# Kernel optimization log

Measured on AMD Instinct MI355X. Metric: run time of the kernel, lower is better.

Reference implementation:

```python
import jax, jax.numpy as jnp
import numpy as np

B, D, H, DOUT, E, K = 8192, 1024, 4096, 1024, 8, 2


def setup_inputs() -> dict:
    key = jax.random.key(0)
    ks = jax.random.split(key, 7)
    s_d = 1.0 / np.sqrt(D)
    s_h = 1.0 / np.sqrt(H)
    return {
        "x": jax.random.normal(ks[0], (B, D), jnp.float32),
        "Wg": jax.random.uniform(ks[1], (D, E), jnp.float32, -s_d, s_d),
        "bg": jax.random.uniform(ks[2], (E,), jnp.float32, -s_d, s_d),
        "W1": jax.random.uniform(ks[3], (E, D, H), jnp.float32, -s_d, s_d),
        "b1": jax.random.uniform(ks[4], (E, H), jnp.float32, -s_d, s_d),
        "W2": jax.random.uniform(ks[5], (E, H, DOUT), jnp.float32, -s_h, s_h),
        "b2": jax.random.uniform(ks[6], (E, DOUT), jnp.float32, -s_h, s_h),
    }


def reference(x, Wg, bg, W1, b1, W2, b2):
    # gating
    gate_probs = jax.nn.softmax(x @ Wg + bg, axis=-1)          # [B, E]
    top_k_probs, top_k_idx = jax.lax.top_k(gate_probs, K)       # [B, K]
    top_k_probs = top_k_probs / jnp.sum(top_k_probs, axis=-1, keepdims=True)

    # dense all-expert compute (faithful to torch.stack over experts)
    h = jax.nn.gelu(jnp.einsum('bd,edh->beh', x, W1) + b1, approximate=False)  # [B, E, H]
    expert_outputs = jnp.einsum('beh,eho->beo', h, W2) + b2                    # [B, E, DOUT]

    # gather selected experts and combine
    sel = jnp.take_along_axis(expert_outputs, top_k_idx[:, :, None], axis=1)   # [B, K, DOUT]
    output = jnp.sum(sel * top_k_probs[:, :, None], axis=1)                    # [B, DOUT]

    # load-balancing aux loss (as written in the original)
    expert_usage = jnp.mean(gate_probs, axis=0)                # [E]
    uniform = jnp.full_like(expert_usage, 1.0 / E)
    aux_loss = jnp.sum(expert_usage * jnp.log(uniform) - jnp.log(expert_usage) * uniform)
    return output, aux_loss
```

## Files before the change

### kernel.cpp

```cpp
#include <hip/hip_runtime.h>
#include <hip/hip_bf16.h>
#include <hip/hip_fp16.h>

#define B_    8192
#define D_    1024
#define H_    4096
#define DOUT_ 1024
#define E_    8
#define MAXR  17408
#define NT256 72

typedef float    f32x4 __attribute__((ext_vector_type(4)));
typedef _Float16 f16x8 __attribute__((ext_vector_type(8)));
typedef unsigned short u16;
typedef u16      u16x8 __attribute__((ext_vector_type(8)));
typedef u16      u16x4 __attribute__((ext_vector_type(4)));
typedef unsigned int u32;

__device__ __forceinline__ u16 f2h_bits(float f) {
  _Float16 h = (_Float16)f;
  return __builtin_bit_cast(u16, h);
}

__device__ __forceinline__ float gelu_f(float v) {
  float z = 0.7978845608028654f * (v + 0.044715f * v * v * v);
  float ez = __expf(2.f * z);
  float th = 1.f - 2.f / (ez + 1.f);
  return 0.5f * v * (1.f + th);
}

#define OFF_TOPI 512
#define OFF_TOPW (OFF_TOPI + 65536)
#define OFF_ATOK (OFF_TOPW + 65536)
#define OFF_WSL  (OFF_ATOK + 69632)
#define OFF_TMAP 280064
#define OFF_XG   524288
#define OFF_W1T  (OFF_XG + 35651584)
#define OFF_W2T  OFF_XG
#define OFF_HB   (OFF_W1T + 67108864)

__global__ void k_zero_out(float* __restrict__ out) {
  size_t i = (size_t)(blockIdx.x * 256 + threadIdx.x) * 4;
  *(f32x4*)&out[i] = (f32x4){0.f, 0.f, 0.f, 0.f};
}

__global__ void k_init(int* __restrict__ atok, float* __restrict__ wslot,
                       int* __restrict__ meta) {
  int i = blockIdx.x * 256 + threadIdx.x;
  if (i < MAXR) { atok[i] = 0; wslot[i] = 0.f; }
  if (blockIdx.x == 0 && threadIdx.x < 64) meta[threadIdx.x] = 0;
}

__global__ __launch_bounds__(256) void k_gate(
    const float* __restrict__ x, const float* __restrict__ Wg,
    const float* __restrict__ bg, int* __restrict__ counts,
    float* __restrict__ usage, int* __restrict__ topi, float* __restrict__ topw) {
  __shared__ float su[E_];
  if (threadIdx.x < E_) su[threadIdx.x] = 0.f;
  __syncthreads();
  const int lane = threadIdx.x & 63;
  const int b = blockIdx.x * 4 + (threadIdx.x >> 6);
  float p[E_] = {0.f,0.f,0.f,0.f,0.f,0.f,0.f,0.f};
  #pragma unroll
  for (int j = 0; j < 4; ++j) {
    int d = j * 256 + lane * 4;
    float4 xv = *(const float4*)&x[(size_t)b * D_ + d];
    const float* wr = &Wg[(size_t)d * E_];
    #pragma unroll
    for (int c = 0; c < 4; ++c) {
      float xc = reinterpret_cast<const float*>(&xv)[c];
      #pragma unroll
      for (int e = 0; e < E_; ++e) p[e] += xc * wr[c * E_ + e];
    }
  }
  #pragma unroll
  for (int off = 32; off >= 1; off >>= 1)
    #pragma unroll
    for (int e = 0; e < E_; ++e) p[e] += __shfl_xor(p[e], off, 64);
  float mx = -1e30f;
  #pragma unroll
  for (int e = 0; e < E_; ++e) { p[e] += bg[e]; mx = fmaxf(mx, p[e]); }
  int i0 = 0; float l0 = p[0];
  #pragma unroll
  for (int e = 1; e < E_; ++e) if (p[e] > l0) { l0 = p[e]; i0 = e; }
  int i1 = -1; float l1 = -1e30f;
  #pragma unroll
  for (int e = 0; e < E_; ++e) if (e != i0 && p[e] > l1) { l1 = p[e]; i1 = e; }
  float s = 0.f;
  #pragma unroll
  for (int e = 0; e < E_; ++e) { p[e] = expf(p[e] - mx); s += p[e]; }
  float inv = 1.f / s;
  if (lane == 0) {
    float e0 = expf(l0 - mx), e1 = expf(l1 - mx);
    float wsum = e0 + e1;
    topi[b * 2] = i0; topi[b * 2 + 1] = i1;
    topw[b * 2] = e0 / wsum; topw[b * 2 + 1] = e1 / wsum;
    atomicAdd(&counts[i0], 1);
    atomicAdd(&counts[i1], 1);
    #pragma unroll
    for (int e = 0; e < E_; ++e) atomicAdd(&su[e], p[e] * inv);
  }
  __syncthreads();
  if (threadIdx.x < E_) atomicAdd(&usage[threadIdx.x], su[threadIdx.x]);
}

__global__ void k_scan_aux(const int* __restrict__ counts, int* __restrict__ offsets,
                           const float* __restrict__ usage, float* __restrict__ auxp,
                           int* __restrict__ tmap) {
  if (threadIdx.x == 0) {
    int off = 0;
    for (int e = 0; e < E_; ++e) { offsets[e] = off; off += (counts[e] + 127) & ~127; }
    offsets[E_] = off;
    int nT = 0;
    for (int e = 0; e < E_; ++e) {
      int roff = offsets[e], pn = offsets[e + 1] - roff;
      for (int r0 = 0; r0 < pn; r0 += 256)
        tmap[nT++] = (e << 20) | (roff + r0);
    }
    for (int t = nT; t < NT256; ++t) tmap[t] = -1;
    float aux = 0.f;
    const float lu = logf(1.0f / (float)E_);
    for (int e = 0; e < E_; ++e) {
      float u = usage[e] * (1.0f / (float)B_);
      aux += u * lu - logf(u) * (1.0f / (float)E_);
    }
    *auxp = aux;
  }
}

__global__ void k_scatter(const int* __restrict__ topi, const float* __restrict__ topw,
                          const int* __restrict__ offsets, int* __restrict__ cursors,
                          int* __restrict__ atok, float* __restrict__ wslot) {
  int b = blockIdx.x * 256 + threadIdx.x;
  if (b >= B_) return;
  #pragma unroll
  for (int k = 0; k < 2; ++k) {
    int e = topi[b * 2 + k];
    int pos = atomicAdd(&cursors[e], 1);
    int slot = offsets[e] + pos;
    atok[slot] = b;
    wslot[slot] = topw[b * 2 + k];
  }
}

__global__ __launch_bounds__(256) void k_gather(const float* __restrict__ x,
                                                const int* __restrict__ atok,
                                                u16* __restrict__ Xg) {
  int slot = blockIdx.x;
  int tok = atok[slot];
  int c = threadIdx.x * 4;
  float4 v = *(const float4*)&x[(size_t)tok * D_ + c];
  const float* vf = reinterpret_cast<const float*>(&v);
  u16x4 o;
  o.x = f2h_bits(vf[0]); o.y = f2h_bits(vf[1]);
  o.z = f2h_bits(vf[2]); o.w = f2h_bits(vf[3]);
  *(u16x4*)&Xg[(size_t)slot * D_ + c] = o;
}

__global__ __launch_bounds__(256) void k_cvt_t(const float* __restrict__ src,
                                               u16* __restrict__ dst, int K, int N) {
  const int e = blockIdx.z;
  const int kt = blockIdx.x * 64;
  const int nt = blockIdx.y * 64;
  __shared__ u16 t[64][68];
  const float* s = src + (size_t)e * K * N;
  u16* d = dst + (size_t)e * N * K;
  const int tr = threadIdx.x >> 4;
  const int tc = threadIdx.x & 15;
  #pragma unroll
  for (int i = 0; i < 4; ++i) {
    int k = tr + i * 16;
    float4 v = *(const float4*)&s[(size_t)(kt + k) * N + nt + tc * 4];
    t[k][tc*4+0] = f2h_bits(v.x); t[k][tc*4+1] = f2h_bits(v.y);
    t[k][tc*4+2] = f2h_bits(v.z); t[k][tc*4+3] = f2h_bits(v.w);
  }
  __syncthreads();
  #pragma unroll
  for (int i = 0; i < 4; ++i) {
    int n = tr + i * 16;
    u16x4 o;
    o.x = t[tc*4+0][n]; o.y = t[tc*4+1][n];
    o.z = t[tc*4+2][n]; o.w = t[tc*4+3][n];
    *(u16x4*)&d[(size_t)(nt + n) * K + kt + tc * 4] = o;
  }
}

#define GLDS(g, l) __builtin_amdgcn_global_load_lds( \
    (const u32 __attribute__((address_space(1)))*)(g), \
    (u32 __attribute__((address_space(3)))*)(l), 16, 0, 0)

#define STG(LDK, kk, Aoff, Boff) do { \
  const int r_ = lane >> 2; \
  const int sc_ = ((lane & 3) ^ ((r_ ^ (r_ >> 2)) & 3)) * 8; \
  _Pragma("unroll") \
  for (int c = 0; c < 2; ++c) { \
    int seg = wid * 2 + c; \
    int rowA = seg * 16 + r_; if (rowA > Alim) rowA = Alim; \
    GLDS(Ap + (size_t)rowA * (LDK) + (kk) + sc_, SM + (Aoff) + seg * 512); \
    GLDS(Bp + (size_t)(seg * 16 + r_) * (LDK) + (kk) + sc_, SM + (Boff) + seg * 512); \
  } } while (0)

#define CMP(Aoff, Boff) do { \
  const int r15_ = lane & 15; \
  const int co_ = (((lane >> 4) ^ ((r15_ ^ (r15_ >> 2)) & 3)) * 8); \
  f16x8 af[8], bf[4]; \
  _Pragma("unroll") \
  for (int m = 0; m < 8; ++m) \
    af[m] = *(const f16x8*)&SM[(Aoff) + (wr * 128 + m * 16 + r15_) * 32 + co_]; \
  _Pragma("unroll") \
  for (int n = 0; n < 4; ++n) \
    bf[n] = *(const f16x8*)&SM[(Boff) + (wc * 64 + n * 16 + r15_) * 32 + co_]; \
  _Pragma("unroll") \
  for (int m = 0; m < 8; ++m) \
    _Pragma("unroll") \
    for (int n = 0; n < 4; ++n) \
      acc[m][n] = __builtin_amdgcn_mfma_f32_16x16x32_f16(af[m], bf[n], acc[m][n], 0, 0, 0); \
  } while (0)

__global__ __launch_bounds__(512, 2) void k_gemm1(
    const u16* __restrict__ Xg, const u16* __restrict__ W1t,
    const float* __restrict__ b1, const int* __restrict__ offsets,
    const int* __restrict__ tmap, u16* __restrict__ Hb) {
  const int packed = tmap[blockIdx.x >> 4];
  if (packed < 0) return;
  const int e = packed >> 20;
  const int row0g = packed & 0xFFFFF;
  const int rend = offsets[e + 1];
  const int nt = blockIdx.x & 15;
  const int n0 = nt * 256;
  const int tid = threadIdx.x, lane = tid & 63, wid = tid >> 6;
  const int wr = wid >> 2, wc = wid & 3;
  const int Alim = (MAXR - 1) - row0g;
  __shared__ __align__(16) u16 SM[32768];
  f32x4 acc[8][4] = {};
  const u16* Ap = Xg + (size_t)row0g * D_;
  const u16* Bp = W1t + (size_t)e * H_ * D_ + (size_t)n0 * D_;

  STG(D_, 0, 0, 8192);
  __syncthreads();
  for (int t = 0; t < 32; t += 2) {
    STG(D_, (t + 1) * 32, 16384, 24576);
    CMP(0, 8192);
    __syncthreads();
    if (t + 2 < 32) STG(D_, (t + 2) * 32, 0, 8192);
    CMP(16384, 24576);
    __syncthreads();
  }
  const int rhi = (lane >> 4) * 4, cix = lane & 15;
  float bv[4];
  #pragma unroll
  for (int n = 0; n < 4; ++n) bv[n] = b1[e * H_ + n0 + wc * 64 + n * 16 + cix];
  #pragma unroll
  for (int rr = 0; rr < 4; ++rr) {
    if (wr == (rr >> 1)) {
      const int mb = (rr & 1) * 4;
      #pragma unroll
      for (int m = 0; m < 4; ++m)
        #pragma unroll
        for (int n = 0; n < 4; ++n)
          #pragma unroll
          for (int j = 0; j < 4; ++j)
            SM[(m * 16 + rhi + j) * 264 + wc * 64 + n * 16 + cix] =
                f2h_bits(gelu_f(acc[mb + m][n][j] + bv[n]));
    }
    __syncthreads();
    {
      const int rl = tid >> 3, co = (tid & 7) * 32;
      const int gr = row0g + rr * 64 + rl;
      if (gr < rend) {
        u16* dst = &Hb[(size_t)gr * H_ + n0 + co];
        const u16* sp = &SM[rl * 264 + co];
        #pragma unroll
        for (int qq = 0; qq < 4; ++qq)
          *(u16x8*)(dst + qq * 8) = *(const u16x8*)(sp + qq * 8);
      }
    }
    __syncthreads();
  }
}

__global__ __launch_bounds__(512, 2) void k_gemm2(
    const u16* __restrict__ Hb, const u16* __restrict__ W2t,
    const float* __restrict__ b2, const int* __restrict__ offsets,
    const int* __restrict__ tmap, const int* __restrict__ atok,
    const float* __restrict__ wslot, float* __restrict__ out) {
  const int packed = tmap[blockIdx.x >> 2];
  if (packed < 0) return;
  const int e = packed >> 20;
  const int row0g = packed & 0xFFFFF;
  const int rend = offsets[e + 1];
  const int nt = blockIdx.x & 3;
  const int n0 = nt * 256;
  const int kbase = blockIdx.y * 2048;
  const int tid = threadIdx.x, lane = tid & 63, wid = tid >> 6;
  const int wr = wid >> 2, wc = wid & 3;
  const int Alim = (MAXR - 1) - row0g;
  __shared__ __align__(16) u16 SM[32768];
  f32x4 acc[8][4] = {};
  const u16* Ap = Hb + (size_t)row0g * H_ + kbase;
  const u16* Bp = W2t + (size_t)e * DOUT_ * H_ + (size_t)n0 * H_ + kbase;

  STG(H_, 0, 0, 8192);
  __syncthreads();
  for (int t = 0; t < 64; t += 2) {
    STG(H_, (t + 1) * 32, 16384, 24576);
    CMP(0, 8192);
    __syncthreads();
    if (t + 2 < 64) STG(H_, (t + 2) * 32, 0, 8192);
    CMP(16384, 24576);
    __syncthreads();
  }
  const int rhi = (lane >> 4) * 4, cix = lane & 15;
  const int first = (kbase == 0);
  float bv[4];
  #pragma unroll
  for (int n = 0; n < 4; ++n) bv[n] = b2[e * DOUT_ + n0 + wc * 64 + n * 16 + cix];
  #pragma unroll
  for (int m = 0; m < 8; ++m) {
    #pragma unroll
    for (int j = 0; j < 4; ++j) {
      int slot = row0g + wr * 128 + m * 16 + rhi + j;
      if (slot >= rend) continue;
      float w = wslot[slot];
      if (w == 0.f) continue;
      int tok = atok[slot];
      float* orow = out + (size_t)tok * DOUT_ + n0;
      #pragma unroll
      for (int n = 0; n < 4; ++n) {
        int lc = wc * 64 + n * 16 + cix;
        float v = first ? w * (acc[m][n][j] + bv[n]) : w * acc[m][n][j];
        atomicAdd(&orow[lc], v);
      }
    }
  }
}

extern "C" void kernel_launch(void* const* d_in, const int* in_sizes, int n_in,
                              void* d_out, int out_size, void* d_ws, size_t ws_size,
                              hipStream_t stream) {
  const float* x  = (const float*)d_in[0];
  const float* Wg = (const float*)d_in[1];
  const float* bg = (const float*)d_in[2];
  const float* W1 = (const float*)d_in[3];
  const float* b1 = (const float*)d_in[4];
  const float* W2 = (const float*)d_in[5];
  const float* b2 = (const float*)d_in[6];
  float* out = (float*)d_out;

  char* ws = (char*)d_ws;
  int*   counts  = (int*)(ws + 0);
  int*   cursors = (int*)(ws + 32);
  int*   offsets = (int*)(ws + 64);
  float* usage   = (float*)(ws + 128);
  int*   topi    = (int*)(ws + OFF_TOPI);
  float* topw    = (float*)(ws + OFF_TOPW);
  int*   atok    = (int*)(ws + OFF_ATOK);
  float* wslot   = (float*)(ws + OFF_WSL);
  int*   tmap    = (int*)(ws + OFF_TMAP);
  u16*   Xg      = (u16*)(ws + OFF_XG);
  u16*   W1t     = (u16*)(ws + OFF_W1T);
  u16*   W2t     = (u16*)(ws + OFF_W2T);
  u16*   Hb      = (u16*)(ws + OFF_HB);

  k_zero_out<<<B_ * DOUT_ / 1024, 256, 0, stream>>>(out);
  k_init<<<(MAXR + 255) / 256, 256, 0, stream>>>(atok, wslot, (int*)ws);
  k_gate<<<B_ / 4, 256, 0, stream>>>(x, Wg, bg, counts, usage, topi, topw);
  k_scan_aux<<<1, 64, 0, stream>>>(counts, offsets, usage, out + (size_t)B_ * DOUT_, tmap);
  k_scatter<<<B_ / 256, 256, 0, stream>>>(topi, topw, offsets, cursors, atok, wslot);
  k_gather<<<MAXR, 256, 0, stream>>>(x, atok, Xg);
  k_cvt_t<<<dim3(D_ / 64, H_ / 64, E_), 256, 0, stream>>>(W1, W1t, D_, H_);
  k_gemm1<<<NT256 * 16, 512, 0, stream>>>(Xg, W1t, b1, offsets, tmap, Hb);
  k_cvt_t<<<dim3(H_ / 64, DOUT_ / 64, E_), 256, 0, stream>>>(W2, W2t, H_, DOUT_);
  k_gemm2<<<dim3(NT256 * 4, 2), 512, 0, stream>>>(Hb, W2t, b2, offsets, tmap, atok, wslot, out);
}
```

Baseline: 963.0 us.

## Deepen GEMM LDS pipeline to four half-stages with explicit vmcnt waits

Doubles shared memory per block to 128KB and restructures both expert GEMM main loops into a two-deep, half-K-step pipeline. Explicit s_waitcnt vmcnt counts replace full __syncthreads drains, so global-to-LDS loads for the next 64-wide K chunk stay in flight while the current one is computed. MFMA sections are also wrapped in s_setprio to favour compute waves. Larger LDS use may reduce occupancy from two blocks per CU, and the hand-counted vmcnt values must match the number of issued loads to remain correct.

```diff
diff --git a/kernel.cpp b/kernel.cpp
--- a/kernel.cpp
+++ b/kernel.cpp
@@ -189,33 +189,49 @@
     (const u32 __attribute__((address_space(1)))*)(g), \
     (u32 __attribute__((address_space(3)))*)(l), 16, 0, 0)
 
-#define STG(LDK, kk, Aoff, Boff) do { \
+#define VMWAIT(N) asm volatile("s_waitcnt vmcnt(" #N ")" ::: "memory")
+#define BARRIER() do { __builtin_amdgcn_s_barrier(); \
+                       asm volatile("" ::: "memory"); } while (0)
+
+#define STGP(LDK, kk, bb, kh) do { \
   const int r_ = lane >> 2; \
   const int sc_ = ((lane & 3) ^ ((r_ ^ (r_ >> 2)) & 3)) * 8; \
   _Pragma("unroll") \
-  for (int c = 0; c < 2; ++c) { \
-    int seg = wid * 2 + c; \
+  for (int j = 0; j < 2; ++j) { \
+    int seg = wid * 2 + j;                        \
     int rowA = seg * 16 + r_; if (rowA > Alim) rowA = Alim; \
-    GLDS(Ap + (size_t)rowA * (LDK) + (kk) + sc_, SM + (Aoff) + seg * 512); \
-    GLDS(Bp + (size_t)(seg * 16 + r_) * (LDK) + (kk) + sc_, SM + (Boff) + seg * 512); \
+    GLDS(Ap + (size_t)rowA * (LDK) + (kk) + (kh) * 32 + sc_, \
+         SM + (bb) + (kh) * 16384 + seg * 512); \
+    GLDS(Bp + (size_t)(seg * 16 + r_) * (LDK) + (kk) + (kh) * 32 + sc_, \
+         SM + (bb) + (kh) * 16384 + 8192 + seg * 512); \
   } } while (0)
 
-#define CMP(Aoff, Boff) do { \
+#define CMPH(bb, kh) do { \
   const int r15_ = lane & 15; \
   const int co_ = (((lane >> 4) ^ ((r15_ ^ (r15_ >> 2)) & 3)) * 8); \
   f16x8 af[8], bf[4]; \
   _Pragma("unroll") \
   for (int m = 0; m < 8; ++m) \
-    af[m] = *(const f16x8*)&SM[(Aoff) + (wr * 128 + m * 16 + r15_) * 32 + co_]; \
+    af[m] = *(const f16x8*)&SM[(bb) + (kh) * 16384 + (wr * 128 + m * 16 + r15_) * 32 + co_]; \
   _Pragma("unroll") \
   for (int n = 0; n < 4; ++n) \
-    bf[n] = *(const f16x8*)&SM[(Boff) + (wc * 64 + n * 16 + r15_) * 32 + co_]; \
+    bf[n] = *(const f16x8*)&SM[(bb) + (kh) * 16384 + 8192 + (wc * 64 + n * 16 + r15_) * 32 + co_]; \
+  __builtin_amdgcn_s_setprio(1); \
   _Pragma("unroll") \
   for (int m = 0; m < 8; ++m) \
     _Pragma("unroll") \
     for (int n = 0; n < 4; ++n) \
       acc[m][n] = __builtin_amdgcn_mfma_f32_16x16x32_f16(af[m], bf[n], acc[m][n], 0, 0, 0); \
+  __builtin_amdgcn_s_setprio(0); \
   } while (0)
+
+#define PHASE(LDK, kk1, nb, cb, kh) do { \
+  STGP(LDK, kk1, nb, kh); \
+  VMWAIT(8); \
+  BARRIER(); \
+  CMPH(cb, kh); \
+  BARRIER(); \
+} while (0)
 
 __global__ __launch_bounds__(512, 2) void k_gemm1(
     const u16* __restrict__ Xg, const u16* __restrict__ W1t,
@@ -231,20 +247,23 @@
   const int tid = threadIdx.x, lane = tid & 63, wid = tid >> 6;
   const int wr = wid >> 2, wc = wid & 3;
   const int Alim = (MAXR - 1) - row0g;
-  __shared__ __align__(16) u16 SM[32768];
+  __shared__ __align__(16) u16 SM[65536];
   f32x4 acc[8][4] = {};
   const u16* Ap = Xg + (size_t)row0g * D_;
   const u16* Bp = W1t + (size_t)e * H_ * D_ + (size_t)n0 * D_;
 
-  STG(D_, 0, 0, 8192);
-  __syncthreads();
-  for (int t = 0; t < 32; t += 2) {
-    STG(D_, (t + 1) * 32, 16384, 24576);
-    CMP(0, 8192);
-    __syncthreads();
-    if (t + 2 < 32) STG(D_, (t + 2) * 32, 0, 8192);
-    CMP(16384, 24576);
-    __syncthreads();
+  STGP(D_, 0, 0, 0);
+  STGP(D_, 0, 0, 1);
+  for (int t = 0; t < 15; ++t) {
+    const int cb = (t & 1) << 15;
+    const int nb = cb ^ 32768;
+    PHASE(D_, (t + 1) * 64, nb, cb, 0);
+    PHASE(D_, (t + 1) * 64, nb, cb, 1);
+  }
+  {
+    const int cb = 32768;
+    VMWAIT(4); BARRIER(); CMPH(cb, 0); BARRIER();
+    VMWAIT(0); BARRIER(); CMPH(cb, 1); BARRIER();
   }
   const int rhi = (lane >> 4) * 4, cix = lane & 15;
   float bv[4];
@@ -295,20 +314,23 @@
   const int tid = threadIdx.x, lane = tid & 63, wid = tid >> 6;
   const int wr = wid >> 2, wc = wid & 3;
   const int Alim = (MAXR - 1) - row0g;
-  __shared__ __align__(16) u16 SM[32768];
+  __shared__ __align__(16) u16 SM[65536];
   f32x4 acc[8][4] = {};
   const u16* Ap = Hb + (size_t)row0g * H_ + kbase;
   const u16* Bp = W2t + (size_t)e * DOUT_ * H_ + (size_t)n0 * H_ + kbase;
 
-  STG(H_, 0, 0, 8192);
-  __syncthreads();
-  for (int t = 0; t < 64; t += 2) {
-    STG(H_, (t + 1) * 32, 16384, 24576);
-    CMP(0, 8192);
-    __syncthreads();
-    if (t + 2 < 64) STG(H_, (t + 2) * 32, 0, 8192);
-    CMP(16384, 24576);
-    __syncthreads();
+  STGP(H_, 0, 0, 0);
+  STGP(H_, 0, 0, 1);
+  for (int t = 0; t < 31; ++t) {
+    const int cb = (t & 1) << 15;
+    const int nb = cb ^ 32768;
+    PHASE(H_, (t + 1) * 64, nb, cb, 0);
+    PHASE(H_, (t + 1) * 64, nb, cb, 1);
+  }
+  {
+    const int cb = 32768;
+    VMWAIT(4); BARRIER(); CMPH(cb, 0); BARRIER();
+    VMWAIT(0); BARRIER(); CMPH(cb, 1); BARRIER();
   }
   const int rhi = (lane >> 4) * 4, cix = lane & 15;
   const int first = (kbase == 0);
```

Result: no change. 960.1 us (-0.3%).
